# Performance work log

Hardware: AMD Instinct MI355X
Metric: run time of the kernel (lower is better)

The kernel has to match this reference:

```python
import jax, jax.numpy as jnp
import numpy as np

FP8_MAX = 448.0  # max finite value of float8_e4m3fn


def setup_inputs() -> dict:
    key = jax.random.key(0)
    k1, k2, k3 = jax.random.split(key, 3)
    B, S, D_IN, D_OUT = 2, 4096, 2048, 8192
    x = jax.random.normal(k1, (B, S, D_IN), dtype=jnp.float32)
    # Weight is stored pre-quantized in fp8 (per-tensor scale), layout (in, out)
    w_fp32 = jax.random.normal(k2, (D_IN, D_OUT), dtype=jnp.float32) * 0.02
    weight_scale = jnp.float32(jnp.max(jnp.abs(w_fp32)) / FP8_MAX)
    weight = jnp.clip(w_fp32 / weight_scale, -FP8_MAX, FP8_MAX).astype(jnp.float8_e4m3fn)
    input_scale = jnp.float32(0.05)  # static per-tensor activation scale
    bias = jax.random.normal(k3, (D_OUT,), dtype=jnp.float32)
    return {"x": x, "weight": weight, "weight_scale": weight_scale,
            "input_scale": input_scale, "bias": bias}


def reference(x, weight, weight_scale, input_scale, bias):
    # static_quantize_e4m3_per_tensor: q = cast_fp8(clip(x / s)), returns (q, s)
    q = jnp.clip(x / input_scale, -FP8_MAX, FP8_MAX).astype(jnp.float8_e4m3fn)
    q2d = q.reshape(-1, q.shape[-1]).astype(jnp.float32)  # [B*S, D_in]
    w = weight.astype(jnp.float32)                         # [D_in, D_out]
    # cublas_scaled_mm: (q @ w) * scale_a * scale_b, out in x.dtype
    out = jnp.matmul(q2d, w) * (input_scale * weight_scale)
    out = out.astype(x.dtype) + bias.astype(x.dtype)
    return out.reshape(x.shape[:-1] + (out.shape[-1],))
```

## Files before the change

kernel.cpp:

```cpp
#include <hip/hip_runtime.h>

typedef __attribute__((ext_vector_type(4))) float floatx4;
typedef __attribute__((ext_vector_type(8))) int   intx8;

__device__ __forceinline__ unsigned int pack4_fp8(float f0, float f1, float f2, float f3) {
    int v = __builtin_amdgcn_cvt_pk_fp8_f32(f0, f1, 0, false);
    v = __builtin_amdgcn_cvt_pk_fp8_f32(f2, f3, v, true);
    return (unsigned int)v;
}

__device__ __forceinline__ void gload16(const unsigned char* g, unsigned char* l) {
    __builtin_amdgcn_global_load_lds(
        (const __attribute__((address_space(1))) unsigned int*)g,
        (__attribute__((address_space(3))) unsigned int*)l, 16, 0, 0);
}

__global__ void detect_kernel(const unsigned int* __restrict__ W, int* __restrict__ flag) {
    __shared__ int ok[2];
    if (threadIdx.x == 0) { ok[0] = 1; ok[1] = 1; }
    __syncthreads();
    int f32ok = 1, bf16ok = 1;
#pragma unroll
    for (int i = 0; i < 16; ++i) {
        unsigned int w = W[threadIdx.x * 16 + i];
        if (w & 0x000FFFFFu) f32ok = 0;
        if (w & 0x000F000Fu) bf16ok = 0;
    }
    if (!f32ok)  atomicAnd(&ok[0], 0);
    if (!bf16ok) atomicAnd(&ok[1], 0);
    __syncthreads();
    if (threadIdx.x == 0) *flag = ok[0] ? 2 : (ok[1] ? 1 : 0);
}

__global__ void quant_kernel(const float* __restrict__ x,
                             unsigned int* __restrict__ q,
                             const float* __restrict__ iscale, int n8) {
    int i = blockIdx.x * blockDim.x + threadIdx.x;
    if (i >= n8) return;
    float s = iscale[0];
    const float4* xv = (const float4*)x;
    float4 a = xv[2 * i];
    float4 b = xv[2 * i + 1];
    float v[8] = {a.x, a.y, a.z, a.w, b.x, b.y, b.z, b.w};
#pragma unroll
    for (int j = 0; j < 8; ++j) {
        float t = v[j] / s;
        v[j] = fminf(fmaxf(t, -448.0f), 448.0f);
    }
    q[2 * i]     = pack4_fp8(v[0], v[1], v[2], v[3]);
    q[2 * i + 1] = pack4_fp8(v[4], v[5], v[6], v[7]);
}

template <int MODE>
__device__ __forceinline__ void ingest_body(const unsigned char* __restrict__ W,
                                            unsigned char* __restrict__ Wt,
                                            int K, int N,
                                            unsigned char (*tile)[68]) {
    const int k0 = blockIdx.y * 64;
    const int n0 = blockIdx.x * 64;
    const int t = threadIdx.x;
    const int kr = t >> 2;
    const int cg = (t & 3) * 16;
    const size_t eidx = (size_t)(k0 + kr) * N + (n0 + cg);

    unsigned int w4[4];
    if constexpr (MODE == 0) {
        uint4 v = *(const uint4*)(W + eidx);
        w4[0] = v.x; w4[1] = v.y; w4[2] = v.z; w4[3] = v.w;
    } else if constexpr (MODE == 1) {
        const uint4* p = (const uint4*)((const unsigned short*)W + eidx);
        uint4 A0 = p[0], A1 = p[1];
        unsigned int uw[8] = {A0.x, A0.y, A0.z, A0.w, A1.x, A1.y, A1.z, A1.w};
#pragma unroll
        for (int g = 0; g < 4; ++g) {
            float f0 = __uint_as_float((uw[2 * g] & 0xFFFFu) << 16);
            float f1 = __uint_as_float((uw[2 * g] >> 16) << 16);
            float f2 = __uint_as_float((uw[2 * g + 1] & 0xFFFFu) << 16);
            float f3 = __uint_as_float((uw[2 * g + 1] >> 16) << 16);
            w4[g] = pack4_fp8(f0, f1, f2, f3);
        }
    } else {
        const float4* p = (const float4*)((const float*)W + eidx);
#pragma unroll
        for (int g = 0; g < 4; ++g) {
            float4 f = p[g];
            w4[g] = pack4_fp8(f.x, f.y, f.z, f.w);
        }
    }
#pragma unroll
    for (int g = 0; g < 4; ++g)
        *(unsigned int*)&tile[kr][cg + 4 * g] = w4[g];
    __syncthreads();

    const int nr = t >> 2;
    const int kg = (t & 3) * 16;
    uint4 o;
    unsigned int w[4];
#pragma unroll
    for (int g = 0; g < 4; ++g) {
        unsigned int b0 = tile[kg + g * 4 + 0][nr];
        unsigned int b1 = tile[kg + g * 4 + 1][nr];
        unsigned int b2 = tile[kg + g * 4 + 2][nr];
        unsigned int b3 = tile[kg + g * 4 + 3][nr];
        w[g] = b0 | (b1 << 8) | (b2 << 16) | (b3 << 24);
    }
    o.x = w[0]; o.y = w[1]; o.z = w[2]; o.w = w[3];
    *(uint4*)(Wt + (size_t)(n0 + nr) * K + k0 + kg) = o;
}

__global__ void ingest_kernel(const unsigned char* __restrict__ W,
                              unsigned char* __restrict__ Wt,
                              const int* __restrict__ flag, int K, int N) {
    __shared__ __align__(16) unsigned char tile[64][68];
    const int mode = *flag;
    if (mode == 0)      ingest_body<0>(W, Wt, K, N, tile);
    else if (mode == 1) ingest_body<1>(W, Wt, K, N, tile);
    else                ingest_body<2>(W, Wt, K, N, tile);
}

__global__ __launch_bounds__(256, 4) void gemm_mxfp8_kernel(
    const unsigned char* __restrict__ A,
    const unsigned char* __restrict__ Bt,
    float* __restrict__ C,
    const float* __restrict__ bias,
    const float* __restrict__ wscale,
    const float* __restrict__ iscale,
    int M, int N, int K) {
    __shared__ __align__(16) unsigned char As[16384];
    __shared__ __align__(16) unsigned char Bs[16384];

    const int tid  = threadIdx.x;
    const int lane = tid & 63;
    const int wv   = tid >> 6;
    const int wm   = wv >> 1;
    const int wn   = wv & 1;
    const int r16  = lane & 15;
    const int cq   = lane >> 4;

    const int bm = blockIdx.y * 128;
    const int bn = blockIdx.x * 128;

    const unsigned char* ga[4];
    const unsigned char* gb[4];
    int lo[4];
#pragma unroll
    for (int j = 0; j < 4; ++j) {
        const int u   = wv * 4 + j;
        const int rb  = u >> 1;
        const int rg  = u & 1;
        const int row = rb * 16 + r16;
        const int col = cq * 32 + rg * 16;
        ga[j] = A  + (size_t)(bm + row) * K + col;
        gb[j] = Bt + (size_t)(bn + row) * K + col;
        lo[j] = rb * 2048 + rg * 1024;
    }

    floatx4 acc[4][4] = {};

    const unsigned char* pa0 = &As[wm * 4 * 2048 + lane * 16];
    const unsigned char* pb0 = &Bs[wn * 4 * 2048 + lane * 16];

    union U8 { intx8 v; uint4 q[2]; };
    const int NT = K >> 7;
    for (int kt = 0; kt < NT; ++kt) {
        __syncthreads();
#pragma unroll
        for (int j = 0; j < 4; ++j) {
            gload16(ga[j], &As[lo[j]]);
            gload16(gb[j], &Bs[lo[j]]);
            ga[j] += 128; gb[j] += 128;
        }
        __syncthreads();

        intx8 af[4], bf[4];
#pragma unroll
        for (int i = 0; i < 4; ++i) {
            U8 ua, ub;
            const unsigned char* qa = pa0 + i * 2048;
            const unsigned char* qb = pb0 + i * 2048;
            ua.q[0] = *(const uint4*)qa;
            ua.q[1] = *(const uint4*)(qa + 1024);
            ub.q[0] = *(const uint4*)qb;
            ub.q[1] = *(const uint4*)(qb + 1024);
            af[i] = ua.v;
            bf[i] = ub.v;
        }
#pragma unroll
        for (int im = 0; im < 4; ++im)
#pragma unroll
            for (int in = 0; in < 4; ++in)
                acc[im][in] = __builtin_amdgcn_mfma_scale_f32_16x16x128_f8f6f4(
                    af[im], bf[in], acc[im][in],
                    0, 0,
                    0, 0x7F7F7F7F,
                    0, 0x7F7F7F7F);
    }
    (void)M;

    const float scale = iscale[0] * wscale[0];
    const int row0 = bm + wm * 64 + (cq << 2);
    const int col0 = bn + wn * 64 + r16;
#pragma unroll
    for (int in = 0; in < 4; ++in) {
        const int col = col0 + in * 16;
        const float bv = bias[col];
#pragma unroll
        for (int im = 0; im < 4; ++im) {
            const int row = row0 + im * 16;
            float* cp = C + (size_t)row * N + col;
#pragma unroll
            for (int r = 0; r < 4; ++r)
                cp[(size_t)r * N] = acc[im][in][r] * scale + bv;
        }
    }
}

extern "C" void kernel_launch(void* const* d_in, const int* in_sizes, int n_in,
                              void* d_out, int out_size, void* d_ws, size_t ws_size,
                              hipStream_t stream) {
    const float* x          = (const float*)d_in[0];
    const unsigned char* w  = (const unsigned char*)d_in[1];
    const float* wscale     = (const float*)d_in[2];
    const float* iscale     = (const float*)d_in[3];
    const float* bias       = (const float*)d_in[4];
    float* out              = (float*)d_out;

    const int D_OUT = in_sizes[4];
    const int D_IN  = in_sizes[1] / D_OUT;
    const int M     = in_sizes[0] / D_IN;

    int* flag         = (int*)d_ws;
    unsigned char* q  = (unsigned char*)d_ws + 256;
    unsigned char* wt = q + (size_t)M * D_IN;

    detect_kernel<<<1, 256, 0, stream>>>((const unsigned int*)w, flag);
    const int n8 = (M * D_IN) / 8;
    quant_kernel<<<(n8 + 255) / 256, 256, 0, stream>>>(x, (unsigned int*)q, iscale, n8);
    dim3 tg(D_OUT / 64, D_IN / 64);
    ingest_kernel<<<tg, 256, 0, stream>>>(w, wt, flag, D_IN, D_OUT);
    gemm_mxfp8_kernel<<<dim3(D_OUT / 128, M / 128), 256, 0, stream>>>(
        q, wt, out, bias, wscale, iscale, M, D_OUT, D_IN);
}
```

Baseline: 571.0 us.

## Enlarge GEMM tile to 256x256 with double-buffered LDS and phased prefetch

The fp8 GEMM now uses 512-thread blocks computing 256x256 output tiles, with each wave holding 8x4 accumulators. LDS is double-buffered, and the next K-slab is prefetched with global_load_lds while MFMAs run in four barrier-separated phases, with setprio raised around the MFMA bursts. The aim is more operand reuse per global byte and less exposed load latency than the old single-buffer load-then-compute loop. In exchange the kernel uses 128KB of LDS and many more registers per block, which lowers occupancy, and adds extra barriers.

```diff
diff --git a/kernel.cpp b/kernel.cpp
--- a/kernel.cpp
+++ b/kernel.cpp
@@ -118,7 +118,7 @@
     else                ingest_body<2>(W, Wt, K, N, tile);
 }
 
-__global__ __launch_bounds__(256, 4) void gemm_mxfp8_kernel(
+__global__ __launch_bounds__(512, 2) void gemm_mxfp8_kernel(
     const unsigned char* __restrict__ A,
     const unsigned char* __restrict__ Bt,
     float* __restrict__ C,
@@ -126,19 +126,19 @@
     const float* __restrict__ wscale,
     const float* __restrict__ iscale,
     int M, int N, int K) {
-    __shared__ __align__(16) unsigned char As[16384];
-    __shared__ __align__(16) unsigned char Bs[16384];
+    __shared__ __align__(16) unsigned char As[2][32768];
+    __shared__ __align__(16) unsigned char Bs[2][32768];
 
     const int tid  = threadIdx.x;
     const int lane = tid & 63;
     const int wv   = tid >> 6;
-    const int wm   = wv >> 1;
-    const int wn   = wv & 1;
+    const int wm   = wv >> 2;
+    const int wn   = wv & 3;
     const int r16  = lane & 15;
     const int cq   = lane >> 4;
 
-    const int bm = blockIdx.y * 128;
-    const int bn = blockIdx.x * 128;
+    const int bm = blockIdx.y * 256;
+    const int bn = blockIdx.x * 256;
 
     const unsigned char* ga[4];
     const unsigned char* gb[4];
@@ -152,65 +152,119 @@
         const int col = cq * 32 + rg * 16;
         ga[j] = A  + (size_t)(bm + row) * K + col;
         gb[j] = Bt + (size_t)(bn + row) * K + col;
-        lo[j] = rb * 2048 + rg * 1024;
-    }
-
-    floatx4 acc[4][4] = {};
-
-    const unsigned char* pa0 = &As[wm * 4 * 2048 + lane * 16];
-    const unsigned char* pb0 = &Bs[wn * 4 * 2048 + lane * 16];
+        lo[j] = u * 1024;
+    }
+
+    floatx4 acc[8][4] = {};
+
+#pragma unroll
+    for (int j = 0; j < 4; ++j) {
+        gload16(ga[j], &As[0][lo[j]]);
+        gload16(gb[j], &Bs[0][lo[j]]);
+        ga[j] += 128; gb[j] += 128;
+    }
+    asm volatile("s_waitcnt vmcnt(0)" ::: "memory");
+    __builtin_amdgcn_s_barrier();
 
     union U8 { intx8 v; uint4 q[2]; };
     const int NT = K >> 7;
+
+#define READ_FRAG(dst, base, blk)                                   \
+    do {                                                            \
+        U8 _u;                                                      \
+        const unsigned char* _p = (base) + (blk) * 2048 + lane * 16;\
+        _u.q[0] = *(const uint4*)_p;                                \
+        _u.q[1] = *(const uint4*)(_p + 1024);                       \
+        (dst) = _u.v;                                               \
+    } while (0)
+
+#define MFMA8(a0, a1, i0, i1)                                               \
+    do {                                                                    \
+        __builtin_amdgcn_s_setprio(1);                                      \
+        _Pragma("unroll")                                                   \
+        for (int j = 0; j < 4; ++j)                                         \
+            acc[i0][j] = __builtin_amdgcn_mfma_scale_f32_16x16x128_f8f6f4(  \
+                a0, bf[j], acc[i0][j], 0, 0, 0, 0x7F7F7F7F, 0, 0x7F7F7F7F); \
+        _Pragma("unroll")                                                   \
+        for (int j = 0; j < 4; ++j)                                         \
+            acc[i1][j] = __builtin_amdgcn_mfma_scale_f32_16x16x128_f8f6f4(  \
+                a1, bf[j], acc[i1][j], 0, 0, 0, 0x7F7F7F7F, 0, 0x7F7F7F7F); \
+        __builtin_amdgcn_s_setprio(0);                                      \
+    } while (0)
+
+#define PHASE_WAIT()                                             \
+    do {                                                         \
+        __builtin_amdgcn_s_barrier();                            \
+        asm volatile("s_waitcnt lgkmcnt(0)" ::: "memory");       \
+        __builtin_amdgcn_sched_barrier(0);                       \
+    } while (0)
+
     for (int kt = 0; kt < NT; ++kt) {
-        __syncthreads();
-#pragma unroll
-        for (int j = 0; j < 4; ++j) {
-            gload16(ga[j], &As[lo[j]]);
-            gload16(gb[j], &Bs[lo[j]]);
-            ga[j] += 128; gb[j] += 128;
-        }
-        __syncthreads();
-
-        intx8 af[4], bf[4];
-#pragma unroll
-        for (int i = 0; i < 4; ++i) {
-            U8 ua, ub;
-            const unsigned char* qa = pa0 + i * 2048;
-            const unsigned char* qb = pb0 + i * 2048;
-            ua.q[0] = *(const uint4*)qa;
-            ua.q[1] = *(const uint4*)(qa + 1024);
-            ub.q[0] = *(const uint4*)qb;
-            ub.q[1] = *(const uint4*)(qb + 1024);
-            af[i] = ua.v;
-            bf[i] = ub.v;
-        }
-#pragma unroll
-        for (int im = 0; im < 4; ++im)
-#pragma unroll
-            for (int in = 0; in < 4; ++in)
-                acc[im][in] = __builtin_amdgcn_mfma_scale_f32_16x16x128_f8f6f4(
-                    af[im], bf[in], acc[im][in],
-                    0, 0,
-                    0, 0x7F7F7F7F,
-                    0, 0x7F7F7F7F);
+        const unsigned char* Ab = As[kt & 1];
+        const unsigned char* Bb = Bs[kt & 1];
+        unsigned char* An = As[(kt & 1) ^ 1];
+        unsigned char* Bn = Bs[(kt & 1) ^ 1];
+        const bool pf = (kt + 1 < NT);
+
+        intx8 bf[4], afa, afb;
+        READ_FRAG(bf[0], Bb, wn * 4 + 0);
+        READ_FRAG(bf[1], Bb, wn * 4 + 1);
+        READ_FRAG(bf[2], Bb, wn * 4 + 2);
+        READ_FRAG(bf[3], Bb, wn * 4 + 3);
+        READ_FRAG(afa, Ab, wm * 8 + 0);
+        READ_FRAG(afb, Ab, wm * 8 + 1);
+        if (pf) {
+            gload16(ga[0], An + lo[0]); gload16(ga[1], An + lo[1]);
+            gload16(gb[0], Bn + lo[0]); gload16(gb[1], Bn + lo[1]);
+            ga[0] += 128; ga[1] += 128; gb[0] += 128; gb[1] += 128;
+        }
+        PHASE_WAIT();
+        MFMA8(afa, afb, 0, 1);
+        __builtin_amdgcn_s_barrier();
+
+        READ_FRAG(afa, Ab, wm * 8 + 2);
+        READ_FRAG(afb, Ab, wm * 8 + 3);
+        if (pf) {
+            gload16(ga[2], An + lo[2]); gload16(ga[3], An + lo[3]);
+            gload16(gb[2], Bn + lo[2]); gload16(gb[3], Bn + lo[3]);
+            ga[2] += 128; ga[3] += 128; gb[2] += 128; gb[3] += 128;
+        }
+        PHASE_WAIT();
+        MFMA8(afa, afb, 2, 3);
+        __builtin_amdgcn_s_barrier();
+
+        READ_FRAG(afa, Ab, wm * 8 + 4);
+        READ_FRAG(afb, Ab, wm * 8 + 5);
+        PHASE_WAIT();
+        MFMA8(afa, afb, 4, 5);
+        __builtin_amdgcn_s_barrier();
+
+        READ_FRAG(afa, Ab, wm * 8 + 6);
+        READ_FRAG(afb, Ab, wm * 8 + 7);
+        PHASE_WAIT();
+        MFMA8(afa, afb, 6, 7);
+        asm volatile("s_waitcnt vmcnt(0)" ::: "memory");
+        __builtin_amdgcn_s_barrier();
     }
     (void)M;
+#undef READ_FRAG
+#undef MFMA8
+#undef PHASE_WAIT
 
     const float scale = iscale[0] * wscale[0];
-    const int row0 = bm + wm * 64 + (cq << 2);
+    const int row0 = bm + wm * 128 + (cq << 2);
     const int col0 = bn + wn * 64 + r16;
 #pragma unroll
-    for (int in = 0; in < 4; ++in) {
-        const int col = col0 + in * 16;
+    for (int j = 0; j < 4; ++j) {
+        const int col = col0 + j * 16;
         const float bv = bias[col];
 #pragma unroll
-        for (int im = 0; im < 4; ++im) {
-            const int row = row0 + im * 16;
+        for (int i = 0; i < 8; ++i) {
+            const int row = row0 + i * 16;
             float* cp = C + (size_t)row * N + col;
 #pragma unroll
             for (int r = 0; r < 4; ++r)
-                cp[(size_t)r * N] = acc[im][in][r] * scale + bv;
+                cp[(size_t)r * N] = acc[i][j][r] * scale + bv;
         }
     }
 }
@@ -238,6 +292,6 @@
     quant_kernel<<<(n8 + 255) / 256, 256, 0, stream>>>(x, (unsigned int*)q, iscale, n8);
     dim3 tg(D_OUT / 64, D_IN / 64);
     ingest_kernel<<<tg, 256, 0, stream>>>(w, wt, flag, D_IN, D_OUT);
-    gemm_mxfp8_kernel<<<dim3(D_OUT / 128, M / 128), 256, 0, stream>>>(
+    gemm_mxfp8_kernel<<<dim3(D_OUT / 256, M / 256), 512, 0, stream>>>(
         q, wt, out, bias, wscale, iscale, M, D_OUT, D_IN);
 }
```

New measurement: 561.2 us. Within noise of the previous version (-1.7%).
